# Kernel tuning notes

Measured on AMD Instinct MI355X. Metric: run time of the kernel, lower is better.

## Reference

```python
import jax, jax.numpy as jnp
import numpy as np


def setup_inputs() -> dict:
    key = jax.random.key(0)
    k1, k2, k3, k4 = jax.random.split(key, 4)
    B, N, F, T, K, O = 16, 1024, 16, 12, 3, 16
    x = jax.random.normal(k1, (B, N, F, T), dtype=jnp.float32)
    spatial_attention = jax.random.uniform(k2, (B, N, N), dtype=jnp.float32)
    adj = jax.random.uniform(k3, (N, N), dtype=jnp.float32)
    # xavier_uniform_ on [K, F, O]: bound = sqrt(6/(F+O)) over last two dims
    bound = float(np.sqrt(6.0 / (F + O)))
    Theta = jax.random.uniform(k4, (K, F, O), dtype=jnp.float32, minval=-bound, maxval=bound)
    return {"x": x, "spatial_attention": spatial_attention, "adj": adj, "Theta": Theta}


def reference(x, spatial_attention, adj, Theta):
    # x: [B, N, F, T], spatial_attention: [B, N, N], adj: [N, N], Theta: [K, F, O]
    B, N, F, T = x.shape
    K = Theta.shape[0]
    a = adj[None, :, :] * spatial_attention                      # [B, N, N]
    eye = jnp.broadcast_to(jnp.eye(N, dtype=x.dtype), (B, N, N))
    supports = [eye, a]
    for _ in range(2, K):                                        # power series of adjacency
        supports.append(jnp.matmul(supports[-1], a))
    S = jnp.stack(supports, axis=0)                              # [K, B, N, N]
    # rhs[k,b,n,f,t] = sum_m S[k,b,m,n] * x[b,m,f,t]  (supports[k]^T @ x), fused over T and K
    rhs = jnp.einsum('kbmn,bmft->kbnft', S, x)                   # [K, B, N, F, T]
    out = jnp.einsum('kbnft,kfo->bnot', rhs, Theta)              # [B, N, O, T]
    return jax.nn.relu(out)
```

## Files before the change

### kernel.cpp

```cpp
#include <hip/hip_runtime.h>
#include <hip/hip_bf16.h>


typedef __attribute__((ext_vector_type(8))) __bf16 bf16x8;
typedef __attribute__((ext_vector_type(4))) float  f32x4;
typedef __attribute__((ext_vector_type(8))) short  short8;

__device__ inline unsigned short f32_to_bf16(float f) {
    unsigned int u = __builtin_bit_cast(unsigned int, f);
    unsigned int r = u + 0x7FFFu + ((u >> 16) & 1u);
    return (unsigned short)(r >> 16);
}
__device__ inline float bf16_to_f32(unsigned short u) {
    unsigned int x = ((unsigned int)u) << 16;
    return __builtin_bit_cast(float, x);
}

__device__ inline void gload_lds16(const void* gsrc, void* ldst) {
    __builtin_amdgcn_global_load_lds(
        (const __attribute__((address_space(1))) unsigned int*)gsrc,
        (__attribute__((address_space(3))) unsigned int*)ldst,
        16, 0, 0);
}

__global__ void prep_a(const float* __restrict__ sa, const float* __restrict__ adj,
                       unsigned short* __restrict__ aT)
{
    __shared__ float tile[32][33];
    const int b  = blockIdx.z;
    const int m0 = blockIdx.y * 32;
    const int n0 = blockIdx.x * 32;
    const int tid = threadIdx.x;
    const int c  = tid & 31;
    const int r4 = tid >> 5;
    const float* sab = sa + (size_t)b * 1024 * 1024;
#pragma unroll
    for (int i = 0; i < 4; i++) {
        int rr = r4 + i * 8;
        size_t idx = (size_t)(m0 + rr) * 1024 + (n0 + c);
        tile[rr][c] = adj[idx] * sab[idx];
    }
    __syncthreads();
    unsigned short* aTb = aT + (size_t)b * 1024 * 1024;
#pragma unroll
    for (int i = 0; i < 4; i++) {
        int rr = r4 + i * 8;
        aTb[(size_t)(n0 + rr) * 1024 + (m0 + c)] = f32_to_bf16(tile[c][rr]);
    }
}

__global__ void prep_x(const float* __restrict__ x, unsigned short* __restrict__ xT)
{
    __shared__ float tile[32][33];
    const int b  = blockIdx.z;
    const int j0 = blockIdx.y * 32;
    const int m0 = blockIdx.x * 32;
    const int tid = threadIdx.x;
    const int c  = tid & 31;
    const int r4 = tid >> 5;
    const float* xb = x + (size_t)b * 1024 * 192;
#pragma unroll
    for (int i = 0; i < 4; i++) {
        int rr = r4 + i * 8;
        tile[rr][c] = xb[(size_t)(m0 + rr) * 192 + (j0 + c)];
    }
    __syncthreads();
    unsigned short* xTb = xT + (size_t)b * 192 * 1024;
#pragma unroll
    for (int i = 0; i < 4; i++) {
        int rr = r4 + i * 8;
        xTb[(size_t)(j0 + rr) * 1024 + (m0 + c)] = f32_to_bf16(tile[c][rr]);
    }
}

__global__ __launch_bounds__(256, 2)
void gemm_tn(const unsigned short* __restrict__ Aop,
             const unsigned short* __restrict__ Bop,
             unsigned short* __restrict__ Cout)
{
    const int b  = blockIdx.z;
    const int j0 = blockIdx.y * 96;
    const int n0 = blockIdx.x * 64;
    const unsigned short* Ab = Aop + (size_t)b * 192 * 1024;
    const unsigned short* Bb = Bop + (size_t)b * 1024 * 1024;

    __shared__ unsigned short Blds[2][64 * 64];

    const int tid  = threadIdx.x;
    const int lane = tid & 63;
    const int wave = tid >> 6;
    const int wj   = wave >> 1;
    const int wn   = wave & 1;
    const int lr   = lane & 15;
    const int lk8  = (lane >> 4) * 8;

    const int srow = lane >> 3;
    const int sg16 = (lane & 7) ^ srow;
    const int sc0  = wave * 2;

    f32x4 acc[3][2];
#pragma unroll
    for (int i = 0; i < 3; i++)
#pragma unroll
        for (int j = 0; j < 2; j++) acc[i][j] = f32x4{0.f, 0.f, 0.f, 0.f};

    const unsigned short* Arow[3];
#pragma unroll
    for (int ri = 0; ri < 3; ri++)
        Arow[ri] = Ab + (size_t)(j0 + wj * 48 + ri * 16 + lr) * 1024 + lk8;

    bf16x8 Ac[2][3], An[2][3];

#pragma unroll
    for (int i = 0; i < 2; i++) {
        int c = sc0 + i;
        gload_lds16(Bb + (size_t)(n0 + 8 * c + srow) * 1024 + sg16 * 8,
                    &Blds[0][c * 512]);
    }
#pragma unroll
    for (int h = 0; h < 2; h++)
#pragma unroll
        for (int ri = 0; ri < 3; ri++)
            Ac[h][ri] = __builtin_bit_cast(bf16x8,
                *reinterpret_cast<const short8*>(Arow[ri] + h * 32));
    __syncthreads();

    int cur = 0;
    for (int t = 0; t < 16; ++t) {
        const int m0 = t * 64;
        if (t < 15) {
#pragma unroll
            for (int i = 0; i < 2; i++) {
                int c = sc0 + i;
                gload_lds16(Bb + (size_t)(n0 + 8 * c + srow) * 1024 + (m0 + 64) + sg16 * 8,
                            &Blds[cur ^ 1][c * 512]);
            }
#pragma unroll
            for (int h = 0; h < 2; h++)
#pragma unroll
                for (int ri = 0; ri < 3; ri++)
                    An[h][ri] = __builtin_bit_cast(bf16x8,
                        *reinterpret_cast<const short8*>(Arow[ri] + m0 + 64 + h * 32));
        }
        bf16x8 Bfr[2][2];
        const char* base = (const char*)&Blds[cur][0];
#pragma unroll
        for (int h = 0; h < 2; h++)
#pragma unroll
            for (int ci = 0; ci < 2; ci++) {
                int row = wn * 32 + ci * 16 + lr;
                int c16 = (h * 32 + lk8) >> 3;
                int sw  = c16 ^ (row & 7);
                Bfr[h][ci] = __builtin_bit_cast(bf16x8,
                    *reinterpret_cast<const short8*>(base + row * 128 + sw * 16));
            }
#pragma unroll
        for (int h = 0; h < 2; h++)
#pragma unroll
            for (int ri = 0; ri < 3; ri++)
#pragma unroll
                for (int ci = 0; ci < 2; ci++)
                    acc[ri][ci] = __builtin_amdgcn_mfma_f32_16x16x32_bf16(
                        Ac[h][ri], Bfr[h][ci], acc[ri][ci], 0, 0, 0);
        __syncthreads();
        if (t < 15) {
#pragma unroll
            for (int h = 0; h < 2; h++)
#pragma unroll
                for (int ri = 0; ri < 3; ri++) Ac[h][ri] = An[h][ri];
            cur ^= 1;
        }
    }

    unsigned short* Cb = Cout + (size_t)b * 192 * 1024;
    const int jw = j0 + wj * 48;
    const int nw = n0 + wn * 32;
#pragma unroll
    for (int ri = 0; ri < 3; ri++)
#pragma unroll
        for (int ci = 0; ci < 2; ci++) {
            int col = nw + ci * 16 + lr;
#pragma unroll
            for (int r = 0; r < 4; r++) {
                int row = jw + ri * 16 + (lane >> 4) * 4 + r;
                Cb[(size_t)row * 1024 + col] = f32_to_bf16(acc[ri][ci][r]);
            }
        }
}

__global__ __launch_bounds__(256)
void final_contract(const unsigned short* __restrict__ xT,
                    const unsigned short* __restrict__ r1,
                    const unsigned short* __restrict__ r2,
                    const float* __restrict__ Theta,
                    float* __restrict__ out)
{
    __shared__ float th[768];
    __shared__ float obuf[64 * 192];

    const int tid = threadIdx.x;
    for (int i = tid; i < 768; i += 256) th[i] = Theta[i];
    __syncthreads();

    const int b  = blockIdx.y;
    const int n0 = blockIdx.x * 64;
    const int nl = tid & 63;
    const int tq = tid >> 6;

    if (tq < 3) {
        float acc[4][16];
#pragma unroll
        for (int tt = 0; tt < 4; tt++)
#pragma unroll
            for (int o = 0; o < 16; o++) acc[tt][o] = 0.f;

        const size_t basep = (size_t)b * 192 * 1024 + n0 + nl;
#pragma unroll
        for (int f = 0; f < 16; f++) {
            size_t off = basep + (size_t)(f * 12 + tq * 4) * 1024;
            float v0[4], v1[4], v2[4];
#pragma unroll
            for (int tt = 0; tt < 4; tt++) {
                v0[tt] = bf16_to_f32(xT[off + (size_t)tt * 1024]);
                v1[tt] = bf16_to_f32(r1[off + (size_t)tt * 1024]);
                v2[tt] = bf16_to_f32(r2[off + (size_t)tt * 1024]);
            }
            const f32x4* t0 = reinterpret_cast<const f32x4*>(&th[0 * 256 + f * 16]);
            const f32x4* t1 = reinterpret_cast<const f32x4*>(&th[1 * 256 + f * 16]);
            const f32x4* t2 = reinterpret_cast<const f32x4*>(&th[2 * 256 + f * 16]);
#pragma unroll
            for (int q = 0; q < 4; q++) {
                f32x4 w0 = t0[q], w1 = t1[q], w2 = t2[q];
#pragma unroll
                for (int tt = 0; tt < 4; tt++)
#pragma unroll
                    for (int e = 0; e < 4; e++)
                        acc[tt][q * 4 + e] += v0[tt] * w0[e] + v1[tt] * w1[e] + v2[tt] * w2[e];
            }
        }
#pragma unroll
        for (int o = 0; o < 16; o++)
#pragma unroll
            for (int tt = 0; tt < 4; tt++)
                obuf[nl * 192 + o * 12 + tq * 4 + tt] = fmaxf(acc[tt][o], 0.f);
    }
    __syncthreads();

    float* outp = out + ((size_t)b * 1024 + n0) * 192;
    const f32x4* src = reinterpret_cast<const f32x4*>(obuf);
    f32x4* dst = reinterpret_cast<f32x4*>(outp);
#pragma unroll
    for (int i = 0; i < 12; i++)
        dst[tid + i * 256] = src[tid + i * 256];
}

extern "C" void kernel_launch(void* const* d_in, const int* in_sizes, int n_in,
                              void* d_out, int out_size, void* d_ws, size_t ws_size,
                              hipStream_t stream)
{
    const float* x     = (const float*)d_in[0];
    const float* sa    = (const float*)d_in[1];
    const float* adj   = (const float*)d_in[2];
    const float* Theta = (const float*)d_in[3];
    float* out = (float*)d_out;

    char* ws = (char*)d_ws;
    const size_t SZ_AT = (size_t)16 * 1024 * 1024 * 2;
    const size_t SZ_XT = (size_t)16 * 192  * 1024 * 2;
    unsigned short* aT = (unsigned short*)ws;
    unsigned short* xT = (unsigned short*)(ws + SZ_AT);
    unsigned short* r1 = (unsigned short*)(ws + SZ_AT + SZ_XT);
    unsigned short* r2 = (unsigned short*)(ws + SZ_AT + 2 * SZ_XT);

    prep_a<<<dim3(32, 32, 16), 256, 0, stream>>>(sa, adj, aT);
    prep_x<<<dim3(32, 6, 16), 256, 0, stream>>>(x, xT);
    gemm_tn<<<dim3(16, 2, 16), 256, 0, stream>>>(xT, aT, r1);
    gemm_tn<<<dim3(16, 2, 16), 256, 0, stream>>>(r1, aT, r2);
    final_contract<<<dim3(16, 16), 256, 0, stream>>>(xT, r1, r2, Theta, out);
}
```

Baseline: 95.57 us.

## Widen GEMM tile to 128 columns with triple-buffered LDS and vmcnt pipelining

The GEMM now uses a 96x128 output tile per block with a three-stage LDS ring for the B operand. It prefetches two stages ahead and replaces __syncthreads with an explicit vmcnt wait plus s_barrier. The final contraction kernel drops its idle wave, pads the LDS output buffer stride, and writes vectorised float4 stores. The goals are more reuse per B load, deeper latency hiding and less bank conflict, at the cost of halving the GEMM grid to 256 blocks and raising register and LDS use per block.

```diff
diff --git a/kernel.cpp b/kernel.cpp
--- a/kernel.cpp
+++ b/kernel.cpp
@@ -73,18 +73,18 @@
     }
 }
 
-__global__ __launch_bounds__(256, 2)
+__global__ __launch_bounds__(256, 1)
 void gemm_tn(const unsigned short* __restrict__ Aop,
              const unsigned short* __restrict__ Bop,
              unsigned short* __restrict__ Cout)
 {
     const int b  = blockIdx.z;
     const int j0 = blockIdx.y * 96;
-    const int n0 = blockIdx.x * 64;
+    const int n0 = blockIdx.x * 128;
     const unsigned short* Ab = Aop + (size_t)b * 192 * 1024;
     const unsigned short* Bb = Bop + (size_t)b * 1024 * 1024;
 
-    __shared__ unsigned short Blds[2][64 * 64];
+    __shared__ unsigned short Blds[3][128 * 64];
 
     const int tid  = threadIdx.x;
     const int lane = tid & 63;
@@ -92,30 +92,35 @@
     const int wj   = wave >> 1;
     const int wn   = wave & 1;
     const int lr   = lane & 15;
-    const int lk8  = (lane >> 4) * 8;
+    const int lg   = lane >> 4;
 
     const int srow = lane >> 3;
     const int sg16 = (lane & 7) ^ srow;
-    const int sc0  = wave * 2;
-
-    f32x4 acc[3][2];
+
+    f32x4 acc[3][4];
 #pragma unroll
     for (int i = 0; i < 3; i++)
 #pragma unroll
-        for (int j = 0; j < 2; j++) acc[i][j] = f32x4{0.f, 0.f, 0.f, 0.f};
+        for (int j = 0; j < 4; j++) acc[i][j] = f32x4{0.f, 0.f, 0.f, 0.f};
 
     const unsigned short* Arow[3];
 #pragma unroll
     for (int ri = 0; ri < 3; ri++)
-        Arow[ri] = Ab + (size_t)(j0 + wj * 48 + ri * 16 + lr) * 1024 + lk8;
+        Arow[ri] = Ab + (size_t)(j0 + wj * 48 + ri * 16 + lr) * 1024 + lg * 8;
 
     bf16x8 Ac[2][3], An[2][3];
 
 #pragma unroll
-    for (int i = 0; i < 2; i++) {
-        int c = sc0 + i;
-        gload_lds16(Bb + (size_t)(n0 + 8 * c + srow) * 1024 + sg16 * 8,
+    for (int i = 0; i < 4; i++) {
+        int c = wave * 4 + i;
+        gload_lds16(Bb + (size_t)(n0 + 8 * c + srow) * 1024 + 0 + sg16 * 8,
                     &Blds[0][c * 512]);
+    }
+#pragma unroll
+    for (int i = 0; i < 4; i++) {
+        int c = wave * 4 + i;
+        gload_lds16(Bb + (size_t)(n0 + 8 * c + srow) * 1024 + 64 + sg16 * 8,
+                    &Blds[1][c * 512]);
     }
 #pragma unroll
     for (int h = 0; h < 2; h++)
@@ -123,72 +128,77 @@
         for (int ri = 0; ri < 3; ri++)
             Ac[h][ri] = __builtin_bit_cast(bf16x8,
                 *reinterpret_cast<const short8*>(Arow[ri] + h * 32));
-    __syncthreads();
-
-    int cur = 0;
+    __builtin_amdgcn_sched_barrier(0);
+    asm volatile("s_waitcnt vmcnt(10)" ::: "memory");
+    __builtin_amdgcn_s_barrier();
+    __builtin_amdgcn_sched_barrier(0);
+
+#pragma unroll
     for (int t = 0; t < 16; ++t) {
-        const int m0 = t * 64;
+        const unsigned short* ldsB = &Blds[t % 3][0];
+        bf16x8 Bfr[2][4];
+#pragma unroll
+        for (int h = 0; h < 2; h++)
+#pragma unroll
+            for (int ci = 0; ci < 4; ci++) {
+                int row = wn * 64 + ci * 16 + lr;
+                int sw  = (h * 4 + lg) ^ (lr & 7);
+                Bfr[h][ci] = __builtin_bit_cast(bf16x8,
+                    *reinterpret_cast<const short8*>(ldsB + row * 64 + sw * 8));
+            }
+        if (t < 14) {
+#pragma unroll
+            for (int i = 0; i < 4; i++) {
+                int c = wave * 4 + i;
+                gload_lds16(Bb + (size_t)(n0 + 8 * c + srow) * 1024 + (t + 2) * 64 + sg16 * 8,
+                            &Blds[(t + 2) % 3][c * 512]);
+            }
+        }
         if (t < 15) {
-#pragma unroll
-            for (int i = 0; i < 2; i++) {
-                int c = sc0 + i;
-                gload_lds16(Bb + (size_t)(n0 + 8 * c + srow) * 1024 + (m0 + 64) + sg16 * 8,
-                            &Blds[cur ^ 1][c * 512]);
-            }
 #pragma unroll
             for (int h = 0; h < 2; h++)
 #pragma unroll
                 for (int ri = 0; ri < 3; ri++)
                     An[h][ri] = __builtin_bit_cast(bf16x8,
-                        *reinterpret_cast<const short8*>(Arow[ri] + m0 + 64 + h * 32));
-        }
-        bf16x8 Bfr[2][2];
-        const char* base = (const char*)&Blds[cur][0];
+                        *reinterpret_cast<const short8*>(Arow[ri] + (t + 1) * 64 + h * 32));
+        }
 #pragma unroll
         for (int h = 0; h < 2; h++)
 #pragma unroll
-            for (int ci = 0; ci < 2; ci++) {
-                int row = wn * 32 + ci * 16 + lr;
-                int c16 = (h * 32 + lk8) >> 3;
-                int sw  = c16 ^ (row & 7);
-                Bfr[h][ci] = __builtin_bit_cast(bf16x8,
-                    *reinterpret_cast<const short8*>(base + row * 128 + sw * 16));
-            }
-#pragma unroll
-        for (int h = 0; h < 2; h++)
-#pragma unroll
             for (int ri = 0; ri < 3; ri++)
 #pragma unroll
-                for (int ci = 0; ci < 2; ci++)
+                for (int ci = 0; ci < 4; ci++)
                     acc[ri][ci] = __builtin_amdgcn_mfma_f32_16x16x32_bf16(
                         Ac[h][ri], Bfr[h][ci], acc[ri][ci], 0, 0, 0);
-        __syncthreads();
-        if (t < 15) {
-#pragma unroll
-            for (int h = 0; h < 2; h++)
-#pragma unroll
-                for (int ri = 0; ri < 3; ri++) Ac[h][ri] = An[h][ri];
-            cur ^= 1;
-        }
+#pragma unroll
+        for (int h = 0; h < 2; h++)
+#pragma unroll
+            for (int ri = 0; ri < 3; ri++)
+                Ac[h][ri] = An[h][ri];
+        asm volatile("s_waitcnt vmcnt(10)" ::: "memory");
+        __builtin_amdgcn_s_barrier();
+        __builtin_amdgcn_sched_barrier(0);
     }
 
     unsigned short* Cb = Cout + (size_t)b * 192 * 1024;
     const int jw = j0 + wj * 48;
-    const int nw = n0 + wn * 32;
+    const int nw = n0 + wn * 64;
 #pragma unroll
     for (int ri = 0; ri < 3; ri++)
 #pragma unroll
-        for (int ci = 0; ci < 2; ci++) {
+        for (int ci = 0; ci < 4; ci++) {
             int col = nw + ci * 16 + lr;
 #pragma unroll
             for (int r = 0; r < 4; r++) {
-                int row = jw + ri * 16 + (lane >> 4) * 4 + r;
+                int row = jw + ri * 16 + lg * 4 + r;
                 Cb[(size_t)row * 1024 + col] = f32_to_bf16(acc[ri][ci][r]);
             }
         }
 }
 
-__global__ __launch_bounds__(256)
+#define OBUF_STRIDE 196
+
+__global__ __launch_bounds__(192)
 void final_contract(const unsigned short* __restrict__ xT,
                     const unsigned short* __restrict__ r1,
                     const unsigned short* __restrict__ r2,
@@ -196,10 +206,10 @@
                     float* __restrict__ out)
 {
     __shared__ float th[768];
-    __shared__ float obuf[64 * 192];
+    __shared__ float obuf[64 * OBUF_STRIDE];
 
     const int tid = threadIdx.x;
-    for (int i = tid; i < 768; i += 256) th[i] = Theta[i];
+    for (int i = tid; i < 768; i += 192) th[i] = Theta[i];
     __syncthreads();
 
     const int b  = blockIdx.y;
@@ -207,51 +217,54 @@
     const int nl = tid & 63;
     const int tq = tid >> 6;
 
-    if (tq < 3) {
-        float acc[4][16];
-#pragma unroll
-        for (int tt = 0; tt < 4; tt++)
-#pragma unroll
-            for (int o = 0; o < 16; o++) acc[tt][o] = 0.f;
-
-        const size_t basep = (size_t)b * 192 * 1024 + n0 + nl;
-#pragma unroll
-        for (int f = 0; f < 16; f++) {
-            size_t off = basep + (size_t)(f * 12 + tq * 4) * 1024;
-            float v0[4], v1[4], v2[4];
-#pragma unroll
-            for (int tt = 0; tt < 4; tt++) {
-                v0[tt] = bf16_to_f32(xT[off + (size_t)tt * 1024]);
-                v1[tt] = bf16_to_f32(r1[off + (size_t)tt * 1024]);
-                v2[tt] = bf16_to_f32(r2[off + (size_t)tt * 1024]);
-            }
-            const f32x4* t0 = reinterpret_cast<const f32x4*>(&th[0 * 256 + f * 16]);
-            const f32x4* t1 = reinterpret_cast<const f32x4*>(&th[1 * 256 + f * 16]);
-            const f32x4* t2 = reinterpret_cast<const f32x4*>(&th[2 * 256 + f * 16]);
-#pragma unroll
-            for (int q = 0; q < 4; q++) {
-                f32x4 w0 = t0[q], w1 = t1[q], w2 = t2[q];
-#pragma unroll
-                for (int tt = 0; tt < 4; tt++)
-#pragma unroll
-                    for (int e = 0; e < 4; e++)
-                        acc[tt][q * 4 + e] += v0[tt] * w0[e] + v1[tt] * w1[e] + v2[tt] * w2[e];
-            }
-        }
-#pragma unroll
-        for (int o = 0; o < 16; o++)
+    float acc[4][16];
+#pragma unroll
+    for (int tt = 0; tt < 4; tt++)
+#pragma unroll
+        for (int o = 0; o < 16; o++) acc[tt][o] = 0.f;
+
+    const size_t basep = (size_t)b * 192 * 1024 + n0 + nl;
+#pragma unroll
+    for (int f = 0; f < 16; f++) {
+        size_t off = basep + (size_t)(f * 12 + tq * 4) * 1024;
+        float v0[4], v1[4], v2[4];
+#pragma unroll
+        for (int tt = 0; tt < 4; tt++) {
+            v0[tt] = bf16_to_f32(xT[off + (size_t)tt * 1024]);
+            v1[tt] = bf16_to_f32(r1[off + (size_t)tt * 1024]);
+            v2[tt] = bf16_to_f32(r2[off + (size_t)tt * 1024]);
+        }
+        const f32x4* t0 = reinterpret_cast<const f32x4*>(&th[0 * 256 + f * 16]);
+        const f32x4* t1 = reinterpret_cast<const f32x4*>(&th[1 * 256 + f * 16]);
+        const f32x4* t2 = reinterpret_cast<const f32x4*>(&th[2 * 256 + f * 16]);
+#pragma unroll
+        for (int q = 0; q < 4; q++) {
+            f32x4 w0 = t0[q], w1 = t1[q], w2 = t2[q];
 #pragma unroll
             for (int tt = 0; tt < 4; tt++)
-                obuf[nl * 192 + o * 12 + tq * 4 + tt] = fmaxf(acc[tt][o], 0.f);
+#pragma unroll
+                for (int e = 0; e < 4; e++)
+                    acc[tt][q * 4 + e] += v0[tt] * w0[e] + v1[tt] * w1[e] + v2[tt] * w2[e];
+        }
+    }
+#pragma unroll
+    for (int o = 0; o < 16; o++) {
+        f32x4 v;
+#pragma unroll
+        for (int tt = 0; tt < 4; tt++) v[tt] = fmaxf(acc[tt][o], 0.f);
+        *reinterpret_cast<f32x4*>(&obuf[nl * OBUF_STRIDE + o * 12 + tq * 4]) = v;
     }
     __syncthreads();
 
     float* outp = out + ((size_t)b * 1024 + n0) * 192;
-    const f32x4* src = reinterpret_cast<const f32x4*>(obuf);
-    f32x4* dst = reinterpret_cast<f32x4*>(outp);
-#pragma unroll
-    for (int i = 0; i < 12; i++)
-        dst[tid + i * 256] = src[tid + i * 256];
+#pragma unroll
+    for (int i = 0; i < 16; i++) {
+        int v   = tid + i * 192;
+        int row = v / 48;
+        int c   = v - row * 48;
+        *reinterpret_cast<f32x4*>(&outp[(size_t)v * 4]) =
+            *reinterpret_cast<const f32x4*>(&obuf[row * OBUF_STRIDE + c * 4]);
+    }
 }
 
 extern "C" void kernel_launch(void* const* d_in, const int* in_sizes, int n_in,
@@ -274,7 +287,7 @@
 
     prep_a<<<dim3(32, 32, 16), 256, 0, stream>>>(sa, adj, aT);
     prep_x<<<dim3(32, 6, 16), 256, 0, stream>>>(x, xT);
-    gemm_tn<<<dim3(16, 2, 16), 256, 0, stream>>>(xT, aT, r1);
-    gemm_tn<<<dim3(16, 2, 16), 256, 0, stream>>>(r1, aT, r2);
-    final_contract<<<dim3(16, 16), 256, 0, stream>>>(xT, r1, r2, Theta, out);
-}
+    gemm_tn<<<dim3(8, 2, 16), 256, 0, stream>>>(xT, aT, r1);
+    gemm_tn<<<dim3(8, 2, 16), 256, 0, stream>>>(r1, aT, r2);
+    final_contract<<<dim3(16, 16), 192, 0, stream>>>(xT, r1, r2, Theta, out);
+}
```

After: 76.62 us. -19.8%, faster.
